# Kernel optimization log

Measured on AMD Instinct MI355X. Metric: run time of the kernel, lower is better.

Reference implementation:

```python
import jax, jax.numpy as jnp
import numpy as np

B, L = 64, 2048
V, E, G = 30, 128, 8          # n_tokens, embedding_size, n_globals
C, F, O = 64, 128, 30         # res_channels, f_channels, n_outputs
K, ND = 2, 9                  # kernel_size, n_dilations
GE = G * E                    # flattened global embedding dim


def causal_conv(x, w, b, dilation):
    # x: [B,Cin,L], w: [Cout,Cin,K] -> [B,Cout,L], causal via left padding
    pad = (w.shape[-1] - 1) * dilation
    out = jax.lax.conv_general_dilated(
        x, w, window_strides=(1,), padding=[(pad, 0)],
        rhs_dilation=(dilation,), dimension_numbers=("NCH", "OIH", "NCH"))
    return out + b[None, :, None]


def setup_inputs() -> dict:
    key = jax.random.key(0)
    ks = jax.random.split(key, 20)
    s = 0.05
    inp = {
        "input_tensor": jax.random.randint(ks[0], (B, L), 0, V),
        "global_input": jax.random.randint(ks[1], (B, G), 0, V),
        "emb_table": jax.random.normal(ks[2], (V, E), jnp.float32) * s,
        "w_causal": jax.random.normal(ks[3], (C, E, K), jnp.float32) * s,
        "b_causal": jnp.zeros((C,), jnp.float32),
        "w_f": jax.random.normal(ks[4], (ND, C, C, K), jnp.float32) * s,
        "b_f": jnp.zeros((ND, C), jnp.float32),
        "w_g": jax.random.normal(ks[5], (ND, C, C, K), jnp.float32) * s,
        "b_g": jnp.zeros((ND, C), jnp.float32),
        "wl_f": jax.random.normal(ks[6], (ND, C, GE), jnp.float32) * s,
        "bl_f": jnp.zeros((ND, C), jnp.float32),
        "wl_g": jax.random.normal(ks[7], (ND, C, GE), jnp.float32) * s,
        "bl_g": jnp.zeros((ND, C), jnp.float32),
        "w_res": jax.random.normal(ks[8], (ND, C, C), jnp.float32) * s,
        "b_res": jnp.zeros((ND, C), jnp.float32),
        "w_fin1": jax.random.normal(ks[9], (F, C), jnp.float32) * s,
        "b_fin1": jnp.zeros((F,), jnp.float32),
        "w_fin2": jax.random.normal(ks[10], (O, F), jnp.float32) * s,
        "b_fin2": jnp.zeros((O,), jnp.float32),
    }
    return inp


def reference(input_tensor, global_input, emb_table, w_causal, b_causal,
              w_f, b_f, w_g, b_g, wl_f, bl_f, wl_g, bl_g,
              w_res, b_res, w_fin1, b_fin1, w_fin2, b_fin2):
    # padding_idx=0: row 0 is zero and receives no gradient
    table = emb_table.at[0].set(0.0)
    emb = table[input_tensor]                     # [B,L,E]
    emb_g = table[global_input].reshape(B, GE)    # [B,G*E]
    x = jnp.transpose(emb, (0, 2, 1))             # [B,E,L]
    res = causal_conv(x, w_causal, b_causal, 1)   # [B,C,L]
    skips = jnp.zeros_like(res)
    for i in range(ND):
        d = 2 ** (i + 1)
        h_f = emb_g @ wl_f[i].T + bl_f[i]         # [B,C]
        h_g = emb_g @ wl_g[i].T + bl_g[i]
        x_f = causal_conv(res, w_f[i], b_f[i], d) + h_f[:, :, None]
        x_g = causal_conv(res, w_g[i], b_g[i], d) + h_g[:, :, None]
        z = jnp.tanh(x_f) * jax.nn.sigmoid(x_g)   # gated activation
        skip = jnp.einsum("oc,bcl->bol", w_res[i], z) + b_res[i][None, :, None]
        res = res + skip
        skips = skips + skip
    out = jax.nn.relu(skips)
    out = jnp.einsum("fc,bcl->bfl", w_fin1, out) + b_fin1[None, :, None]
    out = jax.nn.relu(out)
    out = jnp.einsum("of,bfl->bol", w_fin2, out) + b_fin2[None, :, None]
    return out
```

## Files before the change

### kernel.cpp

```cpp
#include <hip/hip_runtime.h>
#include <stdint.h>

#define Bz 64
#define Lz 2048
#define Vz 30
#define Ez 128
#define Gz 8
#define Cz 64
#define Fz 128
#define Oz 30
#define NDz 9

#define TWOLOG2E 2.8853900817779268f
#define NLOG2E  -1.4426950408889634f

typedef __attribute__((ext_vector_type(8))) short short8;
typedef _Float16 half8 __attribute__((ext_vector_type(8)));
typedef __fp16 fp16x2 __attribute__((ext_vector_type(2)));
typedef __attribute__((ext_vector_type(4))) float floatx4;

#define MFMA16B __builtin_amdgcn_mfma_f32_16x16x32_bf16
#define MFMA16H __builtin_amdgcn_mfma_f32_16x16x32_f16

__device__ __forceinline__ uint16_t f2bf(float f) {
    uint32_t u = __float_as_uint(f);
    u += 0x7fffu + ((u >> 16) & 1u);
    return (uint16_t)(u >> 16);
}
__device__ __forceinline__ uint16_t f2h(float f) {
    return __builtin_bit_cast(uint16_t, (_Float16)f);
}
__device__ __forceinline__ uint32_t pk2h(float lo, float hi) {
    fp16x2 h = __builtin_amdgcn_cvt_pkrtz(lo, hi);
    return __builtin_bit_cast(uint32_t, h);
}
__device__ __forceinline__ uint32_t pkadd(uint32_t oldbits, float a, float b) {
    fp16x2 h = __builtin_bit_cast(fp16x2, oldbits) + __builtin_amdgcn_cvt_pkrtz(a, b);
    return __builtin_bit_cast(uint32_t, h);
}
__device__ __forceinline__ float h2f(uint32_t u16bits) {
    return (float)__builtin_bit_cast(_Float16, (uint16_t)u16bits);
}
__device__ __forceinline__ float fexp2(float x) {
#if __has_builtin(__builtin_amdgcn_exp2f)
    return __builtin_amdgcn_exp2f(x);
#else
    float r; asm("v_exp_f32 %0, %1" : "=v"(r) : "v"(x)); return r;
#endif
}
__device__ __forceinline__ float gatefn(float fl, float gl) {
    float a = fexp2(fl);
    float b = fexp2(gl);
    float ap1 = a + 1.f;
    return (a - 1.f) * __builtin_amdgcn_rcpf(fmaf(ap1, b, ap1));
}

#define N_WB   (NDz * 128 * 128)
#define N_WR   (NDz * 64 * 64)
#define N_W1   (Fz * Cz)
#define N_W2   (32 * Fz)
#define N_PROJ (Vz * Cz)
#define N_WLB  (NDz * 128 * 1024)
#define N_EMB  (Bz * 1024)
#define N_BIAS (NDz * 128)

__global__ void pack_k(const float* __restrict__ w_f, const float* __restrict__ w_g,
                       const float* __restrict__ w_res, const float* __restrict__ w_fin1,
                       const float* __restrict__ w_fin2, const float* __restrict__ w_causal,
                       const float* __restrict__ table, const int* __restrict__ gin,
                       const float* __restrict__ wl_f, const float* __restrict__ wl_g,
                       const float* __restrict__ b_f, const float* __restrict__ b_g,
                       const float* __restrict__ bl_f, const float* __restrict__ bl_g,
                       uint16_t* __restrict__ WB, uint16_t* __restrict__ WrB,
                       uint16_t* __restrict__ W1B, uint16_t* __restrict__ W2B,
                       float* __restrict__ proj0, float* __restrict__ proj1,
                       uint16_t* __restrict__ WLB, uint16_t* __restrict__ embG,
                       float* __restrict__ biasrow) {
    int tid = blockIdx.x * 256 + threadIdx.x;
    if (tid < N_WB) {
        int i = tid >> 14, rem = tid & 16383, ch = rem >> 7, k = rem & 127;
        int kin = k & 63, tap = (k < 64) ? 1 : 0;
        float v = (ch < 64) ? w_f[((i * Cz + ch) * Cz + kin) * 2 + tap] * TWOLOG2E
                            : w_g[((i * Cz + (ch - 64)) * Cz + kin) * 2 + tap] * NLOG2E;
        WB[tid] = f2h(v);
        return;
    }
    tid -= N_WB;
    if (tid < N_WR) { WrB[tid] = f2h(w_res[tid]); return; }
    tid -= N_WR;
    if (tid < N_W1) { W1B[tid] = f2h(w_fin1[tid]); return; }
    tid -= N_W1;
    if (tid < N_W2) {
        int o = tid >> 7, f = tid & 127;
        W2B[tid] = f2h(o < Oz ? w_fin2[o * Fz + f] : 0.f);
        return;
    }
    tid -= N_W2;
    if (tid < N_PROJ) {
        int v = tid >> 6, c = tid & 63;
        float s0 = 0.f, s1 = 0.f;
        if (v != 0) {
            for (int e = 0; e < Ez; e++) {
                float tv = table[v * Ez + e];
                s0 += w_causal[(c * Ez + e) * 2 + 0] * tv;
                s1 += w_causal[(c * Ez + e) * 2 + 1] * tv;
            }
        }
        proj0[tid] = s0; proj1[tid] = s1;
        return;
    }
    tid -= N_PROJ;
    if (tid < N_WLB) {
        int row = tid >> 10, j = tid & 1023;
        int i = row >> 7, rem = row & 127, fg = rem >> 6, c = rem & 63;
        const float* wl = fg ? wl_g : wl_f;
        float sc = fg ? NLOG2E : TWOLOG2E;
        WLB[tid] = f2bf(wl[((size_t)(i * Cz + c)) * 1024 + j] * sc);
        return;
    }
    tid -= N_WLB;
    if (tid < N_EMB) {
        int b = tid >> 10, j = tid & 1023;
        int g = j >> 7, e = j & 127;
        int v = gin[b * Gz + g];
        embG[tid] = f2bf(v ? table[v * Ez + e] : 0.f);
        return;
    }
    tid -= N_EMB;
    if (tid < N_BIAS) {
        int i = tid >> 7, rem = tid & 127, fg = rem >> 6, c = rem & 63;
        float bsum = (fg ? b_g : b_f)[i * Cz + c] + (fg ? bl_g : bl_f)[i * Cz + c];
        biasrow[tid] = bsum * (fg ? NLOG2E : TWOLOG2E);
    }
}

__global__ __launch_bounds__(256) void hgemm_k(
    const uint16_t* __restrict__ WLB, const uint16_t* __restrict__ embG,
    const float* __restrict__ biasrow, float* __restrict__ hhT) {
    __shared__ float red[4][4][64][4];
    int tx = threadIdx.x, lane = tx & 63, wave = tx >> 6;
    int nl = lane & 15, quad = lane >> 4;
    int row0 = blockIdx.x * 16;
    floatx4 acc[4];
#pragma unroll
    for (int nt = 0; nt < 4; nt++)
#pragma unroll
        for (int r = 0; r < 4; r++) acc[nt][r] = 0.f;
    const uint16_t* ap = WLB + (size_t)(row0 + nl) * 1024 + quad * 8;
#pragma unroll
    for (int k8 = 0; k8 < 8; k8++) {
        int ks = wave * 8 + k8;
        short8 a = *(const short8*)(ap + ks * 32);
#pragma unroll
        for (int nt = 0; nt < 4; nt++) {
            short8 bb = *(const short8*)(embG + (size_t)(nt * 16 + nl) * 1024 + ks * 32 + quad * 8);
            acc[nt] = MFMA16B(a, bb, acc[nt], 0, 0, 0);
        }
    }
#pragma unroll
    for (int nt = 0; nt < 4; nt++)
#pragma unroll
        for (int r = 0; r < 4; r++) red[nt][wave][lane][r] = acc[nt][r];
    __syncthreads();
    {
        int nt = wave;
#pragma unroll
        for (int r = 0; r < 4; r++) {
            float s = red[nt][0][lane][r] + red[nt][1][lane][r] +
                      red[nt][2][lane][r] + red[nt][3][lane][r];
            hhT[(size_t)(row0 + quad * 4 + r) * 64 + nt * 16 + nl] =
                s + biasrow[row0 + quad * 4 + r];
        }
    }
}

__global__ __launch_bounds__(256) void init_k(
    const int* __restrict__ tok, const float* __restrict__ b_causal,
    const float* __restrict__ proj0, const float* __restrict__ proj1,
    uint16_t* __restrict__ res) {
    int tx = threadIdx.x;
    int q = tx & 15, tl = tx >> 4;
    int b = blockIdx.y;
    int t = blockIdx.x * 16 + tl;
    int v1 = tok[b * Lz + t];
    int v0 = (t > 0) ? tok[b * Lz + t - 1] : 0;
    float4 p1 = ((const float4*)(proj1 + v1 * Cz))[q];
    float4 p0 = ((const float4*)(proj0 + v0 * Cz))[q];
    float4 bc = ((const float4*)b_causal)[q];
    float rx = p1.x + p0.x + bc.x, ry = p1.y + p0.y + bc.y;
    float rz = p1.z + p0.z + bc.z, rw = p1.w + p0.w + bc.w;
    *(uint2*)(res + ((size_t)(b * Lz + t)) * Cz + q * 4) =
        make_uint2(pk2h(rx, ry), pk2h(rz, rw));
}

__global__ __launch_bounds__(256, 3) void fused_k(
    const uint16_t* __restrict__ rin, uint16_t* __restrict__ rout,
    const uint16_t* __restrict__ WB, const uint16_t* __restrict__ WrB,
    const float* __restrict__ hhT, const float* __restrict__ b_res) {
    __shared__ __align__(16) uint16_t R[192 * 72];
    __shared__ __align__(16) uint16_t Zb[192 * 64];
    int tx = threadIdx.x;
    int lane = tx & 63, wave = tx >> 6;
    int nl = lane & 15, quad = lane >> 4;
    int b = blockIdx.y, t0 = blockIdx.x * 128;
    const uint16_t* rb16 = rin + ((size_t)b * Lz) * Cz;

    if (t0 != 0) {
        const uint16_t* src = rb16 + (size_t)(t0 - 64) * Cz;
#pragma unroll
        for (int it = 0; it < 6; it++) {
            int id = it * 256 + tx, row = id >> 3, c8 = id & 7;
            uint4 v = *(const uint4*)(src + (size_t)row * Cz + c8 * 8);
            *(uint4*)(R + row * 72 + c8 * 8) = v;
        }
    } else {
#pragma unroll
        for (int it = 0; it < 6; it++) {
            int id = it * 256 + tx, row = id >> 3, c8 = id & 7;
            int t = row - 64;
            uint4 v = make_uint4(0u, 0u, 0u, 0u);
            if (t >= 0) v = *(const uint4*)(rb16 + (size_t)t * Cz + c8 * 8);
            *(uint4*)(R + row * 72 + c8 * 8) = v;
        }
    }
    floatx4 ss[8];
#pragma unroll
    for (int j = 0; j < 8; j++)
#pragma unroll
        for (int r = 0; r < 4; r++) ss[j][r] = 0.f;
    __syncthreads();

    const int chq = wave * 16 + quad * 4;
    const int zmask = (nl & 7) << 3;
    const int zwr  = chq ^ zmask;
    const int zrd0 = (quad * 8) ^ zmask;
    const int zrd1 = (quad * 8 + 32) ^ zmask;
    const int NT0[5] = {0, 0, 1, 2, 4};

#pragma unroll
    for (int l = 0; l < 5; l++) {
        const int d = 2 << l;
        const int nt0 = NT0[l];
        const uint16_t* wf = WB + l * 16384 + (wave * 16 + nl) * 128 + quad * 8;
        half8 AF[4], AG[4];
#pragma unroll
        for (int ks = 0; ks < 4; ks++) {
            AF[ks] = *(const half8*)(wf + ks * 32);
            AG[ks] = *(const half8*)(wf + 64 * 128 + ks * 32);
        }
        const uint16_t* wr = WrB + l * 4096 + (wave * 16 + nl) * 64 + quad * 8;
        half8 AR0 = *(const half8*)(wr);
        half8 AR1 = *(const half8*)(wr + 32);
        float hfv[4], hgv[4], brv[4];
        const float* hp = hhT + ((size_t)(l * 128 + wave * 16 + quad * 4)) * 64 + b;
#pragma unroll
        for (int r = 0; r < 4; r++) { hfv[r] = hp[r * 64]; hgv[r] = hp[4096 + r * 64]; }
        const float* brp = b_res + l * Cz + wave * 16 + quad * 4;
#pragma unroll
        for (int r = 0; r < 4; r++) brv[r] = brp[r];

#pragma unroll
        for (int nt = 0; nt < 12; nt++) {
            if (nt < nt0) continue;
            int rowa = nt * 16 + nl;
            int rowb = rowa - d;
            if (nt * 16 < d) rowb = rowb < 0 ? 0 : rowb;
            const uint16_t* ra = R + rowa * 72 + quad * 8;
            const uint16_t* rb = R + rowb * 72 + quad * 8;
            half8 b0 = *(const half8*)(ra);
            half8 b1 = *(const half8*)(ra + 32);
            half8 b2 = *(const half8*)(rb);
            half8 b3 = *(const half8*)(rb + 32);
            floatx4 aF, aG;
#pragma unroll
            for (int r = 0; r < 4; r++) { aF[r] = hfv[r]; aG[r] = hgv[r]; }
            aF = MFMA16H(AF[0], b0, aF, 0, 0, 0); aG = MFMA16H(AG[0], b0, aG, 0, 0, 0);
            aF = MFMA16H(AF[1], b1, aF, 0, 0, 0); aG = MFMA16H(AG[1], b1, aG, 0, 0, 0);
            aF = MFMA16H(AF[2], b2, aF, 0, 0, 0); aG = MFMA16H(AG[2], b2, aG, 0, 0, 0);
            aF = MFMA16H(AF[3], b3, aF, 0, 0, 0); aG = MFMA16H(AG[3], b3, aG, 0, 0, 0);
            float z0 = gatefn(aF[0], aG[0]);
            float z1 = gatefn(aF[1], aG[1]);
            float z2 = gatefn(aF[2], aG[2]);
            float z3 = gatefn(aF[3], aG[3]);
            *(uint2*)(Zb + rowa * 64 + zwr) = make_uint2(pk2h(z0, z1), pk2h(z2, z3));
        }
        __syncthreads();

        if (t0 != 0) {
#pragma unroll
            for (int nt = 0; nt < 12; nt++) {
                if (nt < nt0) continue;
                int pos = nt * 16 + nl;
                const uint16_t* zb0 = Zb + pos * 64;
                floatx4 a2;
#pragma unroll
                for (int r = 0; r < 4; r++) a2[r] = brv[r];
                a2 = MFMA16H(AR0, *(const half8*)(zb0 + zrd0), a2, 0, 0, 0);
                a2 = MFMA16H(AR1, *(const half8*)(zb0 + zrd1), a2, 0, 0, 0);
                uint16_t* rp = R + pos * 72 + chq;
                uint2 oldp = *(uint2*)rp;
                *(uint2*)rp = make_uint2(pkadd(oldp.x, a2[0], a2[1]),
                                         pkadd(oldp.y, a2[2], a2[3]));
                if (nt >= 4) {
#pragma unroll
                    for (int r = 0; r < 4; r++) ss[nt - 4][r] += a2[r];
                }
            }
        } else {
#pragma unroll
            for (int nt = 0; nt < 12; nt++) {
                if (nt < nt0) continue;
                int pos = nt * 16 + nl;
                const uint16_t* zb0 = Zb + pos * 64;
                floatx4 a2;
#pragma unroll
                for (int r = 0; r < 4; r++) a2[r] = brv[r];
                a2 = MFMA16H(AR0, *(const half8*)(zb0 + zrd0), a2, 0, 0, 0);
                a2 = MFMA16H(AR1, *(const half8*)(zb0 + zrd1), a2, 0, 0, 0);
                bool ok = (pos >= 64);
                uint16_t* rp = R + pos * 72 + chq;
                uint2 oldp = *(uint2*)rp;
                uint32_t ux = ok ? pkadd(oldp.x, a2[0], a2[1]) : 0u;
                uint32_t uy = ok ? pkadd(oldp.y, a2[2], a2[3]) : 0u;
                *(uint2*)rp = make_uint2(ux, uy);
                if (nt >= 4) {
#pragma unroll
                    for (int r = 0; r < 4; r++) ss[nt - 4][r] += a2[r];
                }
            }
        }
        __syncthreads();
    }

    uint16_t* ro = rout + ((size_t)b * Lz) * Cz;
#pragma unroll
    for (int j = 0; j < 8; j++) {
        size_t off = (size_t)(t0 + j * 16 + nl) * Cz + chq;
        uint2 rv = *(const uint2*)(rb16 + off);
        *(uint2*)(ro + off) = make_uint2(pkadd(rv.x, ss[j][0], ss[j][1]),
                                         pkadd(rv.y, ss[j][2], ss[j][3]));
    }
}

__global__ __launch_bounds__(256, 2) void pair_k(
    const uint16_t* __restrict__ rin, uint16_t* __restrict__ rout,
    const uint16_t* __restrict__ WB, const uint16_t* __restrict__ WrB,
    const float* __restrict__ hhT, const float* __restrict__ b_res) {
    __shared__ __align__(16) uint16_t R[320 * 72];
    __shared__ __align__(16) uint16_t Zb[256 * 64];
    int tx = threadIdx.x;
    int lane = tx & 63, wave = tx >> 6;
    int nl = lane & 15, quad = lane >> 4;
    int b = blockIdx.y, t0 = blockIdx.x * 128;
    const uint16_t* rb16 = rin + ((size_t)b * Lz) * Cz;

    if (t0 >= 192) {
        const uint16_t* src = rb16 + (size_t)(t0 - 192) * Cz;
#pragma unroll
        for (int it = 0; it < 10; it++) {
            int id = it * 256 + tx, row = id >> 3, c8 = id & 7;
            uint4 v = *(const uint4*)(src + (size_t)row * Cz + c8 * 8);
            *(uint4*)(R + row * 72 + c8 * 8) = v;
        }
    } else {
#pragma unroll
        for (int it = 0; it < 10; it++) {
            int id = it * 256 + tx, row = id >> 3, c8 = id & 7;
            int t = t0 - 192 + row;
            uint4 v = make_uint4(0u, 0u, 0u, 0u);
            if (t >= 0) v = *(const uint4*)(rb16 + (size_t)t * Cz + c8 * 8);
            *(uint4*)(R + row * 72 + c8 * 8) = v;
        }
    }
    __syncthreads();

    const int chq = wave * 16 + quad * 4;
    const int zmask = (nl & 7) << 3;
    const int zwr  = chq ^ zmask;
    const int zrd0 = (quad * 8) ^ zmask;
    const int zrd1 = (quad * 8 + 32) ^ zmask;
    const int thr = 192 - t0;

#pragma unroll
    for (int li = 0; li < 2; li++) {
        const int l = 5 + li;
        const int d = 64 << li;
        const int ntLo = li ? 12 : 4;
        const uint16_t* wf = WB + l * 16384 + (wave * 16 + nl) * 128 + quad * 8;
        half8 AF[4], AG[4];
#pragma unroll
        for (int ks = 0; ks < 4; ks++) {
            AF[ks] = *(const half8*)(wf + ks * 32);
            AG[ks] = *(const half8*)(wf + 64 * 128 + ks * 32);
        }
        const uint16_t* wr = WrB + l * 4096 + (wave * 16 + nl) * 64 + quad * 8;
        half8 AR0 = *(const half8*)(wr);
        half8 AR1 = *(const half8*)(wr + 32);
        float hfv[4], hgv[4], brv[4];
        const float* hp = hhT + ((size_t)(l * 128 + wave * 16 + quad * 4)) * 64 + b;
#pragma unroll
        for (int r = 0; r < 4; r++) { hfv[r] = hp[r * 64]; hgv[r] = hp[4096 + r * 64]; }
        const float* brp = b_res + l * Cz + wave * 16 + quad * 4;
#pragma unroll
        for (int r = 0; r < 4; r++) brv[r] = brp[r];

#pragma unroll
        for (int nt = ntLo; nt < 20; nt++) {
            if (li == 0 && nt * 16 < thr) continue;
            int rowa = nt * 16 + nl;
            int rowb = rowa - d;
            const uint16_t* ra = R + rowa * 72 + quad * 8;
            const uint16_t* rb = R + rowb * 72 + quad * 8;
            half8 b0 = *(const half8*)(ra);
            half8 b1 = *(const half8*)(ra + 32);
            half8 b2 = *(const half8*)(rb);
            half8 b3 = *(const half8*)(rb + 32);
            floatx4 aF, aG;
#pragma unroll
            for (int r = 0; r < 4; r++) { aF[r] = hfv[r]; aG[r] = hgv[r]; }
            aF = MFMA16H(AF[0], b0, aF, 0, 0, 0); aG = MFMA16H(AG[0], b0, aG, 0, 0, 0);
            aF = MFMA16H(AF[1], b1, aF, 0, 0, 0); aG = MFMA16H(AG[1], b1, aG, 0, 0, 0);
            aF = MFMA16H(AF[2], b2, aF, 0, 0, 0); aG = MFMA16H(AG[2], b2, aG, 0, 0, 0);
            aF = MFMA16H(AF[3], b3, aF, 0, 0, 0); aG = MFMA16H(AG[3], b3, aG, 0, 0, 0);
            float z0 = gatefn(aF[0], aG[0]);
            float z1 = gatefn(aF[1], aG[1]);
            float z2 = gatefn(aF[2], aG[2]);
            float z3 = gatefn(aF[3], aG[3]);
            *(uint2*)(Zb + (rowa - 64) * 64 + zwr) = make_uint2(pk2h(z0, z1), pk2h(z2, z3));
        }
        __syncthreads();

#pragma unroll
        for (int nt = ntLo; nt < 20; nt++) {
            if (li == 0 && nt * 16 < thr) continue;
            int pos = nt * 16 + nl;
            const uint16_t* zb0 = Zb + (pos - 64) * 64;
            floatx4 a2;
#pragma unroll
            for (int r = 0; r < 4; r++) a2[r] = brv[r];
            a2 = MFMA16H(AR0, *(const half8*)(zb0 + zrd0), a2, 0, 0, 0);
            a2 = MFMA16H(AR1, *(const half8*)(zb0 + zrd1), a2, 0, 0, 0);
            uint16_t* rp = R + pos * 72 + chq;
            uint2 oldp = *(uint2*)rp;
            *(uint2*)rp = make_uint2(pkadd(oldp.x, a2[0], a2[1]),
                                     pkadd(oldp.y, a2[2], a2[3]));
        }
        __syncthreads();
    }

    uint16_t* ro = rout + ((size_t)b * Lz) * Cz;
#pragma unroll
    for (int j = 0; j < 8; j++) {
        int s = 192 + j * 16 + nl;
        size_t off = (size_t)(t0 + j * 16 + nl) * Cz + chq;
        *(uint2*)(ro + off) = *(const uint2*)(R + s * 72 + chq);
    }
}

__global__ __launch_bounds__(256, 4) void layer_k(
    const uint16_t* __restrict__ rin, uint16_t* __restrict__ rout,
    const uint16_t* __restrict__ WBl, const uint16_t* __restrict__ WrBl,
    const float* __restrict__ hhT, const float* __restrict__ b_res,
    int i, int d) {
    __shared__ __align__(16) uint16_t X[64 * 136];
    __shared__ __align__(16) uint16_t Z[64 * 72];
    int tx = threadIdx.x;
    int lane = tx & 63, wave = tx >> 6;
    int nl = lane & 15, quad = lane >> 4;
    int b = blockIdx.y, t0 = blockIdx.x * 64;
    const uint16_t* rb16 = rin + ((size_t)b * Lz) * Cz;

#pragma unroll
    for (int it = 0; it < 2; it++) {
        int id = it * 256 + tx, row = id >> 3, c8 = id & 7;
        uint4 v = *(const uint4*)(rb16 + (size_t)(t0 + row) * Cz + c8 * 8);
        *(uint4*)(X + row * 136 + c8 * 8) = v;
    }
#pragma unroll
    for (int it = 0; it < 2; it++) {
        int id = it * 256 + tx, row = id >> 3, c8 = id & 7;
        int tb = t0 + row - d;
        uint4 v = make_uint4(0u, 0u, 0u, 0u);
        if (tb >= 0) v = *(const uint4*)(rb16 + (size_t)tb * Cz + c8 * 8);
        *(uint4*)(X + row * 136 + 64 + c8 * 8) = v;
    }

    half8 AF[4], AG[4], AR[2];
    {
        const uint16_t* wf = WBl + (wave * 16 + nl) * 128 + quad * 8;
#pragma unroll
        for (int ks = 0; ks < 4; ks++) {
            AF[ks] = *(const half8*)(wf + ks * 32);
            AG[ks] = *(const half8*)(wf + 64 * 128 + ks * 32);
        }
        const uint16_t* wr = WrBl + (wave * 16 + nl) * 64 + quad * 8;
#pragma unroll
        for (int ks = 0; ks < 2; ks++) AR[ks] = *(const half8*)(wr + ks * 32);
    }
    float hfv[4], hgv[4], brv[4];
    {
        const float* hp = hhT + ((size_t)(i * 128 + wave * 16 + quad * 4)) * 64 + b;
#pragma unroll
        for (int r = 0; r < 4; r++) {
            hfv[r] = hp[r * 64];
            hgv[r] = hp[4096 + r * 64];
        }
        const float* brp = b_res + i * Cz + wave * 16 + quad * 4;
#pragma unroll
        for (int r = 0; r < 4; r++) brv[r] = brp[r];
    }
    __syncthreads();

    floatx4 accF[4], accG[4];
#pragma unroll
    for (int nt = 0; nt < 4; nt++)
#pragma unroll
        for (int r = 0; r < 4; r++) { accF[nt][r] = hfv[r]; accG[nt][r] = hgv[r]; }
#pragma unroll
    for (int nt = 0; nt < 4; nt++) {
        const uint16_t* xp = X + (nt * 16 + nl) * 136 + quad * 8;
#pragma unroll
        for (int ks = 0; ks < 4; ks++) {
            half8 bf = *(const half8*)(xp + ks * 32);
            accF[nt] = MFMA16H(AF[ks], bf, accF[nt], 0, 0, 0);
            accG[nt] = MFMA16H(AG[ks], bf, accG[nt], 0, 0, 0);
        }
    }

    int chq = wave * 16 + quad * 4;
#pragma unroll
    for (int nt = 0; nt < 4; nt++) {
        int pos = nt * 16 + nl;
        float z0 = gatefn(accF[nt][0], accG[nt][0]);
        float z1 = gatefn(accF[nt][1], accG[nt][1]);
        float z2 = gatefn(accF[nt][2], accG[nt][2]);
        float z3 = gatefn(accF[nt][3], accG[nt][3]);
        *(uint2*)(Z + pos * 72 + chq) = make_uint2(pk2h(z0, z1), pk2h(z2, z3));
    }
    __syncthreads();

    floatx4 acc2[4];
#pragma unroll
    for (int nt = 0; nt < 4; nt++)
#pragma unroll
        for (int r = 0; r < 4; r++) acc2[nt][r] = brv[r];
#pragma unroll
    for (int nt = 0; nt < 4; nt++) {
        const uint16_t* zp = Z + (nt * 16 + nl) * 72 + quad * 8;
        acc2[nt] = MFMA16H(AR[0], *(const half8*)zp, acc2[nt], 0, 0, 0);
        acc2[nt] = MFMA16H(AR[1], *(const half8*)(zp + 32), acc2[nt], 0, 0, 0);
    }

    uint16_t* ro = rout + ((size_t)b * Lz) * Cz;
#pragma unroll
    for (int nt = 0; nt < 4; nt++) {
        size_t off = (size_t)(t0 + nt * 16 + nl) * Cz + chq;
        uint2 rv = *(const uint2*)(rb16 + off);
        *(uint2*)(ro + off) = make_uint2(pkadd(rv.x, acc2[nt][0], acc2[nt][1]),
                                         pkadd(rv.y, acc2[nt][2], acc2[nt][3]));
    }
}

__global__ __launch_bounds__(256, 3) void final_k(
    const uint16_t* __restrict__ res0, const uint16_t* __restrict__ resF,
    const uint16_t* __restrict__ W1B, const uint16_t* __restrict__ W2B,
    const float* __restrict__ b_fin1, const float* __restrict__ b_fin2,
    float* __restrict__ out) {
    __shared__ __align__(16) uint16_t S[128 * 72];
    __shared__ __align__(16) uint16_t Mi[128 * 136];
    int tx = threadIdx.x;
    int lane = tx & 63, wave = tx >> 6;
    int nl = lane & 15, quad = lane >> 4;
    int b = blockIdx.y, t0 = blockIdx.x * 128;
    const uint16_t* r0 = res0 + ((size_t)b * Lz) * Cz;
    const uint16_t* rF = resF + ((size_t)b * Lz) * Cz;

    half8 A1[2][2], A2[2][4];
#pragma unroll
    for (int mt = 0; mt < 2; mt++) {
        const uint16_t* w1 = W1B + (wave * 32 + mt * 16 + nl) * 64 + quad * 8;
#pragma unroll
        for (int ks = 0; ks < 2; ks++) A1[mt][ks] = *(const half8*)(w1 + ks * 32);
        const uint16_t* w2 = W2B + (mt * 16 + nl) * 128 + quad * 8;
#pragma unroll
        for (int ks = 0; ks < 4; ks++) A2[mt][ks] = *(const half8*)(w2 + ks * 32);
    }
#pragma unroll
    for (int it = 0; it < 4; it++) {
        int id = it * 256 + tx, row = id >> 3, c8 = id & 7;
        uint4 fv = *(const uint4*)(rF + (size_t)(t0 + row) * Cz + c8 * 8);
        uint4 ov = *(const uint4*)(r0 + (size_t)(t0 + row) * Cz + c8 * 8);
        float s0 = fmaxf(h2f(fv.x) - h2f(ov.x), 0.f);
        float s1 = fmaxf(h2f(fv.x >> 16) - h2f(ov.x >> 16), 0.f);
        float s2 = fmaxf(h2f(fv.y) - h2f(ov.y), 0.f);
        float s3 = fmaxf(h2f(fv.y >> 16) - h2f(ov.y >> 16), 0.f);
        float s4 = fmaxf(h2f(fv.z) - h2f(ov.z), 0.f);
        float s5 = fmaxf(h2f(fv.z >> 16) - h2f(ov.z >> 16), 0.f);
        float s6 = fmaxf(h2f(fv.w) - h2f(ov.w), 0.f);
        float s7 = fmaxf(h2f(fv.w >> 16) - h2f(ov.w >> 16), 0.f);
        *(uint4*)(S + row * 72 + c8 * 8) =
            make_uint4(pk2h(s0, s1), pk2h(s2, s3), pk2h(s4, s5), pk2h(s6, s7));
    }
    __syncthreads();

    floatx4 accM[2][8];
    float b1v[2][4];
#pragma unroll
    for (int mt = 0; mt < 2; mt++)
#pragma unroll
        for (int r = 0; r < 4; r++) b1v[mt][r] = b_fin1[wave * 32 + mt * 16 + quad * 4 + r];
#pragma unroll
    for (int mt = 0; mt < 2; mt++)
#pragma unroll
        for (int nt = 0; nt < 8; nt++)
#pragma unroll
            for (int r = 0; r < 4; r++) accM[mt][nt][r] = b1v[mt][r];
#pragma unroll
    for (int nt = 0; nt < 8; nt++) {
        const uint16_t* sp = S + (nt * 16 + nl) * 72 + quad * 8;
#pragma unroll
        for (int ks = 0; ks < 2; ks++) {
            half8 s = *(const half8*)(sp + ks * 32);
            accM[0][nt] = MFMA16H(A1[0][ks], s, accM[0][nt], 0, 0, 0);
            accM[1][nt] = MFMA16H(A1[1][ks], s, accM[1][nt], 0, 0, 0);
        }
    }
#pragma unroll
    for (int mt = 0; mt < 2; mt++)
#pragma unroll
        for (int nt = 0; nt < 8; nt++) {
            int pos = nt * 16 + nl;
            int fq = wave * 32 + mt * 16 + quad * 4;
            float m0 = fmaxf(accM[mt][nt][0], 0.f), m1 = fmaxf(accM[mt][nt][1], 0.f);
            float m2 = fmaxf(accM[mt][nt][2], 0.f), m3 = fmaxf(accM[mt][nt][3], 0.f);
            *(uint2*)(Mi + pos * 136 + fq) = make_uint2(pk2h(m0, m1), pk2h(m2, m3));
        }
    __syncthreads();

    floatx4 accO[2][2];
#pragma unroll
    for (int mt = 0; mt < 2; mt++)
#pragma unroll
        for (int r = 0; r < 4; r++) {
            int o = mt * 16 + quad * 4 + r;
            float bo = (o < Oz) ? b_fin2[o] : 0.f;
            accO[mt][0][r] = bo; accO[mt][1][r] = bo;
        }
#pragma unroll
    for (int ntl = 0; ntl < 2; ntl++) {
        int nt = wave * 2 + ntl;
        const uint16_t* mp = Mi + (nt * 16 + nl) * 136 + quad * 8;
#pragma unroll
        for (int ks = 0; ks < 4; ks++) {
            half8 m = *(const half8*)(mp + ks * 32);
            accO[0][ntl] = MFMA16H(A2[0][ks], m, accO[0][ntl], 0, 0, 0);
            accO[1][ntl] = MFMA16H(A2[1][ks], m, accO[1][ntl], 0, 0, 0);
        }
    }
#pragma unroll
    for (int mt = 0; mt < 2; mt++)
#pragma unroll
        for (int ntl = 0; ntl < 2; ntl++)
#pragma unroll
            for (int r = 0; r < 4; r++) {
                int o = mt * 16 + quad * 4 + r;
                if (o < Oz)
                    out[((size_t)b * Oz + o) * Lz + t0 + (wave * 2 + ntl) * 16 + nl] =
                        accO[mt][ntl][r];
            }
}

extern "C" void kernel_launch(void* const* d_in, const int* in_sizes, int n_in,
                              void* d_out, int out_size, void* d_ws, size_t ws_size,
                              hipStream_t stream) {
    const int*   tok      = (const int*)d_in[0];
    const int*   gin      = (const int*)d_in[1];
    const float* table    = (const float*)d_in[2];
    const float* w_causal = (const float*)d_in[3];
    const float* b_causal = (const float*)d_in[4];
    const float* w_f      = (const float*)d_in[5];
    const float* b_f      = (const float*)d_in[6];
    const float* w_g      = (const float*)d_in[7];
    const float* b_g      = (const float*)d_in[8];
    const float* wl_f     = (const float*)d_in[9];
    const float* bl_f     = (const float*)d_in[10];
    const float* wl_g     = (const float*)d_in[11];
    const float* bl_g     = (const float*)d_in[12];
    const float* w_res    = (const float*)d_in[13];
    const float* b_res    = (const float*)d_in[14];
    const float* w_fin1   = (const float*)d_in[15];
    const float* b_fin1   = (const float*)d_in[16];
    const float* w_fin2   = (const float*)d_in[17];
    const float* b_fin2   = (const float*)d_in[18];
    float* out = (float*)d_out;

    const size_t NRES = (size_t)Bz * Lz * Cz;
    uint16_t* u16 = (uint16_t*)d_ws;
    uint16_t* resA = u16;
    uint16_t* resB = resA + NRES;
    uint16_t* resC = resB + NRES;
    uint16_t* WB   = resC + NRES;
    uint16_t* WrB  = WB + N_WB;
    uint16_t* W1B  = WrB + N_WR;
    uint16_t* W2B  = W1B + N_W1;
    uint16_t* WLB  = W2B + N_W2;
    uint16_t* embG = WLB + N_WLB;
    float* hhT     = (float*)(embG + N_EMB);
    float* proj0   = hhT + 73728;
    float* proj1   = proj0 + N_PROJ;
    float* biasrow = proj1 + N_PROJ;

    int npack = N_WB + N_WR + N_W1 + N_W2 + N_PROJ + N_WLB + N_EMB + N_BIAS;
    pack_k<<<(npack + 255) / 256, 256, 0, stream>>>(
        w_f, w_g, w_res, w_fin1, w_fin2, w_causal, table, gin,
        wl_f, wl_g, b_f, b_g, bl_f, bl_g,
        WB, WrB, W1B, W2B, proj0, proj1, WLB, embG, biasrow);
    hgemm_k<<<72, 256, 0, stream>>>(WLB, embG, biasrow, hhT);
    init_k<<<dim3(Lz / 16, Bz), 256, 0, stream>>>(tok, b_causal, proj0, proj1, resA);

    fused_k<<<dim3(Lz / 128, Bz), 256, 0, stream>>>(resA, resB, WB, WrB, hhT, b_res);
    pair_k<<<dim3(Lz / 128, Bz), 256, 0, stream>>>(resB, resC, WB, WrB, hhT, b_res);
    layer_k<<<dim3(Lz / 64, Bz), 256, 0, stream>>>(
        resC, resB, WB + (size_t)7 * 16384, WrB + (size_t)7 * 4096, hhT, b_res, 7, 256);
    layer_k<<<dim3(Lz / 64, Bz), 256, 0, stream>>>(
        resB, resC, WB + (size_t)8 * 16384, WrB + (size_t)8 * 4096, hhT, b_res, 8, 512);
    final_k<<<dim3(Lz / 128, Bz), 256, 0, stream>>>(resA, resC, W1B, W2B,
                                                    b_fin1, b_fin2, out);
}
```

Baseline: 262.9 us.

## Fuse last dilated layer into final output head kernel

```diff
diff --git a/kernel.cpp b/kernel.cpp
--- a/kernel.cpp
+++ b/kernel.cpp
@@ -561,62 +561,127 @@
     }
 }
 
-__global__ __launch_bounds__(256, 3) void final_k(
-    const uint16_t* __restrict__ res0, const uint16_t* __restrict__ resF,
+__global__ __launch_bounds__(256, 3) void final8_k(
+    const uint16_t* __restrict__ res0, const uint16_t* __restrict__ res7,
+    const uint16_t* __restrict__ WBl, const uint16_t* __restrict__ WrBl,
+    const float* __restrict__ hhT, const float* __restrict__ b_res,
     const uint16_t* __restrict__ W1B, const uint16_t* __restrict__ W2B,
     const float* __restrict__ b_fin1, const float* __restrict__ b_fin2,
     float* __restrict__ out) {
-    __shared__ __align__(16) uint16_t S[128 * 72];
-    __shared__ __align__(16) uint16_t Mi[128 * 136];
+    __shared__ __align__(16) uint16_t X[64 * 136];
+    __shared__ __align__(16) uint16_t Z[64 * 72];
+    __shared__ __align__(16) uint16_t S[64 * 72];
+    __shared__ __align__(16) uint16_t Mi[64 * 136];
+    const int d = 512;
     int tx = threadIdx.x;
     int lane = tx & 63, wave = tx >> 6;
     int nl = lane & 15, quad = lane >> 4;
-    int b = blockIdx.y, t0 = blockIdx.x * 128;
+    int b = blockIdx.y, t0 = blockIdx.x * 64;
+    const uint16_t* r7 = res7 + ((size_t)b * Lz) * Cz;
     const uint16_t* r0 = res0 + ((size_t)b * Lz) * Cz;
-    const uint16_t* rF = resF + ((size_t)b * Lz) * Cz;
-
-    half8 A1[2][2], A2[2][4];
+
+#pragma unroll
+    for (int it = 0; it < 2; it++) {
+        int id = it * 256 + tx, row = id >> 3, c8 = id & 7;
+        uint4 v = *(const uint4*)(r7 + (size_t)(t0 + row) * Cz + c8 * 8);
+        *(uint4*)(X + row * 136 + c8 * 8) = v;
+    }
+#pragma unroll
+    for (int it = 0; it < 2; it++) {
+        int id = it * 256 + tx, row = id >> 3, c8 = id & 7;
+        int tb = t0 + row - d;
+        uint4 v = make_uint4(0u, 0u, 0u, 0u);
+        if (tb >= 0) v = *(const uint4*)(r7 + (size_t)tb * Cz + c8 * 8);
+        *(uint4*)(X + row * 136 + 64 + c8 * 8) = v;
+    }
+
+    half8 AF[4], AG[4], AR[2];
+    {
+        const uint16_t* wf = WBl + (wave * 16 + nl) * 128 + quad * 8;
+#pragma unroll
+        for (int ks = 0; ks < 4; ks++) {
+            AF[ks] = *(const half8*)(wf + ks * 32);
+            AG[ks] = *(const half8*)(wf + 64 * 128 + ks * 32);
+        }
+        const uint16_t* wr = WrBl + (wave * 16 + nl) * 64 + quad * 8;
+#pragma unroll
+        for (int ks = 0; ks < 2; ks++) AR[ks] = *(const half8*)(wr + ks * 32);
+    }
+    float hfv[4], hgv[4], brv[4];
+    {
+        const float* hp = hhT + ((size_t)(8 * 128 + wave * 16 + quad * 4)) * 64 + b;
+#pragma unroll
+        for (int r = 0; r < 4; r++) {
+            hfv[r] = hp[r * 64];
+            hgv[r] = hp[4096 + r * 64];
+        }
+        const float* brp = b_res + 8 * Cz + wave * 16 + quad * 4;
+#pragma unroll
+        for (int r = 0; r < 4; r++) brv[r] = brp[r];
+    }
+    __syncthreads();
+
+    int chq = wave * 16 + quad * 4;
+#pragma unroll
+    for (int nt = 0; nt < 4; nt++) {
+        const uint16_t* xp = X + (nt * 16 + nl) * 136 + quad * 8;
+        floatx4 aF, aG;
+#pragma unroll
+        for (int r = 0; r < 4; r++) { aF[r] = hfv[r]; aG[r] = hgv[r]; }
+#pragma unroll
+        for (int ks = 0; ks < 4; ks++) {
+            half8 bf = *(const half8*)(xp + ks * 32);
+            aF = MFMA16H(AF[ks], bf, aF, 0, 0, 0);
+            aG = MFMA16H(AG[ks], bf, aG, 0, 0, 0);
+        }
+        int pos = nt * 16 + nl;
+        float z0 = gatefn(aF[0], aG[0]);
+        float z1 = gatefn(aF[1], aG[1]);
+        float z2 = gatefn(aF[2], aG[2]);
+        float z3 = gatefn(aF[3], aG[3]);
+        *(uint2*)(Z + pos * 72 + chq) = make_uint2(pk2h(z0, z1), pk2h(z2, z3));
+    }
+    __syncthreads();
+
+#pragma unroll
+    for (int nt = 0; nt < 4; nt++) {
+        int pos = nt * 16 + nl;
+        const uint16_t* zp = Z + pos * 72 + quad * 8;
+        floatx4 a2;
+#pragma unroll
+        for (int r = 0; r < 4; r++) a2[r] = brv[r];
+        a2 = MFMA16H(AR[0], *(const half8*)zp, a2, 0, 0, 0);
+        a2 = MFMA16H(AR[1], *(const half8*)(zp + 32), a2, 0, 0, 0);
+        uint2 xv = *(const uint2*)(X + pos * 136 + chq);
+        uint2 ov = *(const uint2*)(r0 + (size_t)(t0 + pos) * Cz + chq);
+        float s0 = fmaxf(h2f(xv.x)       + a2[0] - h2f(ov.x),       0.f);
+        float s1 = fmaxf(h2f(xv.x >> 16) + a2[1] - h2f(ov.x >> 16), 0.f);
+        float s2 = fmaxf(h2f(xv.y)       + a2[2] - h2f(ov.y),       0.f);
+        float s3 = fmaxf(h2f(xv.y >> 16) + a2[3] - h2f(ov.y >> 16), 0.f);
+        *(uint2*)(S + pos * 72 + chq) = make_uint2(pk2h(s0, s1), pk2h(s2, s3));
+    }
+    __syncthreads();
+
+    half8 A1[2][2];
 #pragma unroll
     for (int mt = 0; mt < 2; mt++) {
         const uint16_t* w1 = W1B + (wave * 32 + mt * 16 + nl) * 64 + quad * 8;
 #pragma unroll
         for (int ks = 0; ks < 2; ks++) A1[mt][ks] = *(const half8*)(w1 + ks * 32);
-        const uint16_t* w2 = W2B + (mt * 16 + nl) * 128 + quad * 8;
-#pragma unroll
-        for (int ks = 0; ks < 4; ks++) A2[mt][ks] = *(const half8*)(w2 + ks * 32);
-    }
-#pragma unroll
-    for (int it = 0; it < 4; it++) {
-        int id = it * 256 + tx, row = id >> 3, c8 = id & 7;
-        uint4 fv = *(const uint4*)(rF + (size_t)(t0 + row) * Cz + c8 * 8);
-        uint4 ov = *(const uint4*)(r0 + (size_t)(t0 + row) * Cz + c8 * 8);
-        float s0 = fmaxf(h2f(fv.x) - h2f(ov.x), 0.f);
-        float s1 = fmaxf(h2f(fv.x >> 16) - h2f(ov.x >> 16), 0.f);
-        float s2 = fmaxf(h2f(fv.y) - h2f(ov.y), 0.f);
-        float s3 = fmaxf(h2f(fv.y >> 16) - h2f(ov.y >> 16), 0.f);
-        float s4 = fmaxf(h2f(fv.z) - h2f(ov.z), 0.f);
-        float s5 = fmaxf(h2f(fv.z >> 16) - h2f(ov.z >> 16), 0.f);
-        float s6 = fmaxf(h2f(fv.w) - h2f(ov.w), 0.f);
-        float s7 = fmaxf(h2f(fv.w >> 16) - h2f(ov.w >> 16), 0.f);
-        *(uint4*)(S + row * 72 + c8 * 8) =
-            make_uint4(pk2h(s0, s1), pk2h(s2, s3), pk2h(s4, s5), pk2h(s6, s7));
-    }
-    __syncthreads();
-
-    floatx4 accM[2][8];
-    float b1v[2][4];
-#pragma unroll
-    for (int mt = 0; mt < 2; mt++)
-#pragma unroll
-        for (int r = 0; r < 4; r++) b1v[mt][r] = b_fin1[wave * 32 + mt * 16 + quad * 4 + r];
-#pragma unroll
-    for (int mt = 0; mt < 2; mt++)
-#pragma unroll
-        for (int nt = 0; nt < 8; nt++)
-#pragma unroll
-            for (int r = 0; r < 4; r++) accM[mt][nt][r] = b1v[mt][r];
-#pragma unroll
-    for (int nt = 0; nt < 8; nt++) {
+    }
+    floatx4 accM[2][4];
+#pragma unroll
+    for (int mt = 0; mt < 2; mt++) {
+        float b1v[4];
+#pragma unroll
+        for (int r = 0; r < 4; r++) b1v[r] = b_fin1[wave * 32 + mt * 16 + quad * 4 + r];
+#pragma unroll
+        for (int nt = 0; nt < 4; nt++)
+#pragma unroll
+            for (int r = 0; r < 4; r++) accM[mt][nt][r] = b1v[r];
+    }
+#pragma unroll
+    for (int nt = 0; nt < 4; nt++) {
         const uint16_t* sp = S + (nt * 16 + nl) * 72 + quad * 8;
 #pragma unroll
         for (int ks = 0; ks < 2; ks++) {
@@ -628,7 +693,7 @@
 #pragma unroll
     for (int mt = 0; mt < 2; mt++)
 #pragma unroll
-        for (int nt = 0; nt < 8; nt++) {
+        for (int nt = 0; nt < 4; nt++) {
             int pos = nt * 16 + nl;
             int fq = wave * 32 + mt * 16 + quad * 4;
             float m0 = fmaxf(accM[mt][nt][0], 0.f), m1 = fmaxf(accM[mt][nt][1], 0.f);
@@ -637,37 +702,38 @@
         }
     __syncthreads();
 
-    floatx4 accO[2][2];
+    half8 A2[2][4];
+#pragma unroll
+    for (int mt = 0; mt < 2; mt++) {
+        const uint16_t* w2 = W2B + (mt * 16 + nl) * 128 + quad * 8;
+#pragma unroll
+        for (int ks = 0; ks < 4; ks++) A2[mt][ks] = *(const half8*)(w2 + ks * 32);
+    }
+    floatx4 accO[2];
 #pragma unroll
     for (int mt = 0; mt < 2; mt++)
 #pragma unroll
         for (int r = 0; r < 4; r++) {
             int o = mt * 16 + quad * 4 + r;
-            float bo = (o < Oz) ? b_fin2[o] : 0.f;
-            accO[mt][0][r] = bo; accO[mt][1][r] = bo;
-        }
-#pragma unroll
-    for (int ntl = 0; ntl < 2; ntl++) {
-        int nt = wave * 2 + ntl;
-        const uint16_t* mp = Mi + (nt * 16 + nl) * 136 + quad * 8;
+            accO[mt][r] = (o < Oz) ? b_fin2[o] : 0.f;
+        }
+    {
+        const uint16_t* mp = Mi + (wave * 16 + nl) * 136 + quad * 8;
 #pragma unroll
         for (int ks = 0; ks < 4; ks++) {
             half8 m = *(const half8*)(mp + ks * 32);
-            accO[0][ntl] = MFMA16H(A2[0][ks], m, accO[0][ntl], 0, 0, 0);
-            accO[1][ntl] = MFMA16H(A2[1][ks], m, accO[1][ntl], 0, 0, 0);
+            accO[0] = MFMA16H(A2[0][ks], m, accO[0], 0, 0, 0);
+            accO[1] = MFMA16H(A2[1][ks], m, accO[1], 0, 0, 0);
         }
     }
 #pragma unroll
     for (int mt = 0; mt < 2; mt++)
 #pragma unroll
-        for (int ntl = 0; ntl < 2; ntl++)
-#pragma unroll
-            for (int r = 0; r < 4; r++) {
-                int o = mt * 16 + quad * 4 + r;
-                if (o < Oz)
-                    out[((size_t)b * Oz + o) * Lz + t0 + (wave * 2 + ntl) * 16 + nl] =
-                        accO[mt][ntl][r];
-            }
+        for (int r = 0; r < 4; r++) {
+            int o = mt * 16 + quad * 4 + r;
+            if (o < Oz)
+                out[((size_t)b * Oz + o) * Lz + t0 + wave * 16 + nl] = accO[mt][r];
+        }
 }
 
 extern "C" void kernel_launch(void* const* d_in, const int* in_sizes, int n_in,
@@ -722,8 +788,7 @@
     pair_k<<<dim3(Lz / 128, Bz), 256, 0, stream>>>(resB, resC, WB, WrB, hhT, b_res);
     layer_k<<<dim3(Lz / 64, Bz), 256, 0, stream>>>(
         resC, resB, WB + (size_t)7 * 16384, WrB + (size_t)7 * 4096, hhT, b_res, 7, 256);
-    layer_k<<<dim3(Lz / 64, Bz), 256, 0, stream>>>(
-        resB, resC, WB + (size_t)8 * 16384, WrB + (size_t)8 * 4096, hhT, b_res, 8, 512);
-    final_k<<<dim3(Lz / 128, Bz), 256, 0, stream>>>(resA, resC, W1B, W2B,
-                                                    b_fin1, b_fin2, out);
-}
+    final8_k<<<dim3(Lz / 64, Bz), 256, 0, stream>>>(
+        resA, resB, WB + (size_t)8 * 16384, WrB + (size_t)8 * 4096, hhT, b_res,
+        W1B, W2B, b_fin1, b_fin2, out);
+}
```

New measurement: 264.2 us. Within noise of the previous version (+0.5%).
